# Kernel optimization log

Measured on AMD Instinct MI355X. Metric: run time of the kernel, lower is better.

The kernel has to match this reference:

```python
import jax, jax.numpy as jnp
import numpy as np

N_IN = 512
N_OUT = 256
T = 2048
B = 32


def setup_inputs() -> dict:
    key = jax.random.key(0)
    ks = jax.random.split(key, 9)
    s_in = 1.0 / np.sqrt(N_IN)
    inp = {
        "xt": jax.random.normal(ks[0], (T, B, N_IN), dtype=jnp.float32),
        "ct_forward": jax.random.normal(ks[1], (1, B, N_OUT), dtype=jnp.float32),
        # weights stored torch-style as [out, in]
        "Wx": jax.random.uniform(ks[2], (N_OUT, N_IN), jnp.float32, -s_in, s_in),
        "Wf": jax.random.uniform(ks[3], (N_OUT, N_IN), jnp.float32, -s_in, s_in),
        "bf": jax.random.uniform(ks[4], (N_OUT,), jnp.float32, -s_in, s_in),
        "Wr": jax.random.uniform(ks[5], (N_OUT, N_IN), jnp.float32, -s_in, s_in),
        "br": jax.random.uniform(ks[6], (N_OUT,), jnp.float32, -s_in, s_in),
        "Wc": jax.random.uniform(ks[7], (N_OUT, N_IN), jnp.float32, -s_in, s_in),
        "bc": jax.random.uniform(ks[8], (N_OUT,), jnp.float32, -s_in, s_in),
    }
    return inp


def reference(xt, ct_forward, Wx, Wf, bf, Wr, br, Wc, bc):
    # Batched projections over all timesteps (the GEMM part of SRU).
    x_proj = jnp.einsum("tbi,oi->tbo", xt, Wx)              # [T,B,n_out]
    f = jax.nn.sigmoid(jnp.einsum("tbi,oi->tbo", xt, Wf) + bf)
    r = jax.nn.sigmoid(jnp.einsum("tbi,oi->tbo", xt, Wr) + br)
    cx = jnp.einsum("tbi,oi->tbo", xt, Wc) + bc

    def step(c, inp):
        x_t, ft, rt, cxt = inp
        c = ft * c + (1.0 - ft) * x_t
        h = rt * jnp.tanh(c) + (1.0 - rt) * cxt
        return c, h

    c_final, ht = jax.lax.scan(step, ct_forward[0], (x_proj, f, r, cx))
    # dropout=0.0 -> identity; forward returns (ht, ct)
    return ht, c_final
```

## Files before the change

kernel.cpp:

```cpp
#include <hip/hip_runtime.h>
#include <stdint.h>

#define T_STEPS 2048
#define BATCH   32
#define NIN     512
#define NOUT    256
#define MROWS   (T_STEPS*BATCH)
#define BO      (BATCH*NOUT)
#define NCHUNK  32
#define CHLEN   (T_STEPS/NCHUNK)

typedef _Float16 f16x8 __attribute__((ext_vector_type(8)));
typedef _Float16 f16x4 __attribute__((ext_vector_type(4)));
typedef float    fx4   __attribute__((ext_vector_type(4)));

#define LDSP(p) ((__attribute__((address_space(3))) void*)(p))
#define GLBP(p) ((const __attribute__((address_space(1))) void*)(p))

#define BAR()        asm volatile("s_barrier" ::: "memory")
#define WAITLGKM0()  do { asm volatile("s_waitcnt lgkmcnt(0)" ::: "memory"); __builtin_amdgcn_sched_barrier(0); } while(0)
#define WAITVM(n)    do { asm volatile("s_waitcnt vmcnt(" #n ")" ::: "memory"); __builtin_amdgcn_sched_barrier(0); } while(0)

__global__ __launch_bounds__(256) void convert_w(
    const float* __restrict__ Wx, const float* __restrict__ Wf,
    const float* __restrict__ Wr, const float* __restrict__ Wc,
    _Float16* __restrict__ Wcat)
{
    int idx = blockIdx.x * 256 + threadIdx.x;
    int n  = idx >> 7;
    int k4 = (idx & 127) * 4;
    int g = n >> 8, o = n & 255;
    const float* W = (g == 0) ? Wx : (g == 1) ? Wf : (g == 2) ? Wr : Wc;
    float4 v = *(const float4*)(W + o * NIN + k4);
    f16x4 h;
    h[0] = (_Float16)v.x; h[1] = (_Float16)v.y;
    h[2] = (_Float16)v.z; h[3] = (_Float16)v.w;
    *(f16x4*)(Wcat + n * NIN + k4) = h;
}

#define BM 256
#define BN 256
#define BK 64
#define NGT 32

__global__ __launch_bounds__(512, 1) void gemm_proj(
    const float*    __restrict__ xt,
    const _Float16* __restrict__ Wcat,
    const float* __restrict__ bfv, const float* __restrict__ brv, const float* __restrict__ bcv,
    _Float16* __restrict__ xp_h, _Float16* __restrict__ f_h,
    _Float16* __restrict__ r_h,  _Float16* __restrict__ cx_h)
{
    __shared__ char lds[131072];

    const int tid  = threadIdx.x;
    const int lane = tid & 63;
    const int w    = tid >> 6;
    const int wrq  = w >> 2;
    const int wcq  = w & 3;
    const int lr = lane & 15, lk = lane >> 4;

    int wg = (blockIdx.x & 7) * 32 + (blockIdx.x >> 3);
    const int  cg   = wg & 3;
    const int  mgrp = wg >> 2;
    const long m0 = (long)mgrp * 1024;
    const int  n0 = cg * BN;

    const char* baseAg = (const char*)xt + (m0 + (tid >> 4)) * 2048 + (tid & 15) * 16;
    const int awbase = (tid >> 4) * 128 + (((tid & 15) * 8) ^ (((tid >> 4) & 7) << 4));

    const int rl8  = lane >> 3;
    const int scol = (((lane & 7) ^ rl8) << 4);
    const char* baseB = (const char*)Wcat + ((long)(n0 + w * 8 + rl8)) * 1024 + scol;

    float4 av_h0[4], av_h1[4];
#define ALOAD_H(gi, half, dst) do {                                          \
        const char* _b = baseAg + (long)((gi) >> 3) * 524288                 \
                         + ((gi) & 7) * 256 + (half) * 262144;               \
        _Pragma("unroll")                                                    \
        for (int jj = 0; jj < 4; ++jj)                                       \
            dst[jj] = *(const float4*)(_b + jj * 65536);                     \
    } while (0)
#define AWRITE_H(gi, half, src) do {                                         \
        char* _d = lds + ((gi) & 1) * 32768 + (half) * 16384 + awbase;       \
        _Pragma("unroll")                                                    \
        for (int jj = 0; jj < 4; ++jj) {                                     \
            f16x4 _h;                                                        \
            _h[0] = (_Float16)src[jj].x; _h[1] = (_Float16)src[jj].y;        \
            _h[2] = (_Float16)src[jj].z; _h[3] = (_Float16)src[jj].w;        \
            *(f16x4*)(_d + jj * 4096) = _h;                                  \
        }                                                                    \
    } while (0)
#define STAGE_B(g, h) do {                                                   \
        char* _d = lds + 65536 + ((g) & 1) * 32768 + (h) * 16384 + w * 1024; \
        const char* _s = baseB + ((g) & 7) * 128 + (long)(h) * 131072;       \
        __builtin_amdgcn_global_load_lds(GLBP(_s),         LDSP(_d),        16, 0, 0); \
        __builtin_amdgcn_global_load_lds(GLBP(_s + 65536), LDSP(_d + 8192), 16, 0, 0); \
    } while (0)

    fx4 acc[2][2][4][2];
    #pragma unroll
    for (int a = 0; a < 2; ++a)
        #pragma unroll
        for (int b = 0; b < 2; ++b)
            #pragma unroll
            for (int c = 0; c < 4; ++c)
                #pragma unroll
                for (int d = 0; d < 2; ++d)
                    acc[a][b][c][d] = (fx4){0.f, 0.f, 0.f, 0.f};

    f16x8 Ar[4][2];
    f16x8 B0r[2][2];
    f16x8 B1r[2][2];

#define READ_A(c2, h) do {                                                   \
        _Pragma("unroll")                                                    \
        for (int mf = 0; mf < 4; ++mf) {                                     \
            int rl = wrq * 64 + mf * 16 + lr;                                \
            int rb = (c2) * 32768 + (h) * 16384 + rl * 128;                  \
            _Pragma("unroll")                                                \
            for (int kk = 0; kk < 2; ++kk)                                   \
                Ar[mf][kk] = *(const f16x8*)(lds + rb +                      \
                    ((kk * 64 + lk * 16) ^ ((rl & 7) << 4)));                \
        }                                                                    \
    } while (0)
#define READ_B(c2, h, dst) do {                                              \
        _Pragma("unroll")                                                    \
        for (int nf = 0; nf < 2; ++nf) {                                     \
            int rl = wcq * 32 + nf * 16 + lr;                                \
            int rb = 65536 + (c2) * 32768 + (h) * 16384 + rl * 128;          \
            _Pragma("unroll")                                                \
            for (int kk = 0; kk < 2; ++kk)                                   \
                dst[nf][kk] = *(const f16x8*)(lds + rb +                     \
                    ((kk * 64 + lk * 16) ^ ((rl & 7) << 4)));                \
        }                                                                    \
    } while (0)
#define MMACC(Qr, Qc, Br) do {                                               \
        __builtin_amdgcn_s_setprio(1);                                       \
        _Pragma("unroll")                                                    \
        for (int kk = 0; kk < 2; ++kk)                                       \
            _Pragma("unroll")                                                \
            for (int mf = 0; mf < 4; ++mf)                                   \
                _Pragma("unroll")                                            \
                for (int nf = 0; nf < 2; ++nf)                               \
                    acc[Qr][Qc][mf][nf] = __builtin_amdgcn_mfma_f32_16x16x32_f16( \
                        Br[nf][kk], Ar[mf][kk], acc[Qr][Qc][mf][nf], 0, 0, 0);    \
        __builtin_amdgcn_s_setprio(0);                                       \
    } while (0)

    const int g_out = cg;
    _Float16* outp = (g_out == 0) ? xp_h : (g_out == 1) ? f_h : (g_out == 2) ? r_h : cx_h;
    const float* bias = (g_out == 1) ? bfv : (g_out == 2) ? brv : (g_out == 3) ? bcv : nullptr;

    ALOAD_H(0, 0, av_h0); ALOAD_H(0, 1, av_h1);
    STAGE_B(0, 0); STAGE_B(0, 1);
    WAITVM(4);
    AWRITE_H(0, 0, av_h0); AWRITE_H(0, 1, av_h1);
    ALOAD_H(1, 0, av_h0); ALOAD_H(1, 1, av_h1);
    WAITVM(8);
    WAITLGKM0();
    BAR();

    for (int g = 0; g < NGT; ++g) {
        const int c2 = g & 1;
        READ_A(c2, 0);
        READ_B(c2, 0, B0r);
        if (g + 1 < NGT) STAGE_B(g + 1, 0);
        WAITLGKM0();
        MMACC(0, 0, B0r);
        READ_B(c2, 1, B1r);
        if (g + 1 < NGT) STAGE_B(g + 1, 1);
        WAITLGKM0();
        MMACC(0, 1, B1r);
        READ_A(c2, 1);
        WAITLGKM0();
        MMACC(1, 0, B0r);
        MMACC(1, 1, B1r);
        WAITVM(0);
        if (g + 1 < NGT) {
            AWRITE_H(g + 1, 0, av_h0);
            AWRITE_H(g + 1, 1, av_h1);
            if (g + 2 < NGT) {
                ALOAD_H(g + 2, 0, av_h0);
                ALOAD_H(g + 2, 1, av_h1);
            }
        }
        WAITLGKM0();
        BAR();
        if ((g & 7) == 7) {
            const long mbase = m0 + (long)(g >> 3) * 256;
            #pragma unroll
            for (int Qr = 0; Qr < 2; ++Qr) {
                #pragma unroll
                for (int Qc = 0; Qc < 2; ++Qc) {
                    #pragma unroll
                    for (int nf = 0; nf < 2; ++nf) {
                        const int ob = Qc * 128 + wcq * 32 + nf * 16 + lk * 4;
                        float4 bv4 = (g_out == 0) ? (float4){0.f, 0.f, 0.f, 0.f}
                                                  : *(const float4*)(bias + ob);
                        #pragma unroll
                        for (int mf = 0; mf < 4; ++mf) {
                            long row = mbase + Qr * 128 + wrq * 64 + mf * 16 + lr;
                            fx4 v = acc[Qr][Qc][mf][nf];
                            f16x4 hv;
                            if (g_out == 1 || g_out == 2) {
                                float p0 = v[0] + bv4.x, p1 = v[1] + bv4.y;
                                float p2 = v[2] + bv4.z, p3 = v[3] + bv4.w;
                                hv[0] = (_Float16)(__builtin_amdgcn_rcpf(1.0f + __expf(-p0)));
                                hv[1] = (_Float16)(__builtin_amdgcn_rcpf(1.0f + __expf(-p1)));
                                hv[2] = (_Float16)(__builtin_amdgcn_rcpf(1.0f + __expf(-p2)));
                                hv[3] = (_Float16)(__builtin_amdgcn_rcpf(1.0f + __expf(-p3)));
                            } else {
                                hv[0] = (_Float16)(v[0] + bv4.x);
                                hv[1] = (_Float16)(v[1] + bv4.y);
                                hv[2] = (_Float16)(v[2] + bv4.z);
                                hv[3] = (_Float16)(v[3] + bv4.w);
                            }
                            *(f16x4*)(outp + row * NOUT + ob) = hv;
                            acc[Qr][Qc][mf][nf] = (fx4){0.f, 0.f, 0.f, 0.f};
                        }
                    }
                }
            }
        }
    }
}

__global__ __launch_bounds__(256) void chunk_scan_a(
    const _Float16* __restrict__ f_h, const _Float16* __restrict__ xp_h,
    float* __restrict__ chunkA, float* __restrict__ chunkB)
{
    int tid2 = blockIdx.x * 256 + threadIdx.x;
    int ch = tid2 >> 11;
    int b4 = (tid2 & 2047) << 2;
    long base = (long)ch * CHLEN * BO + b4;
    fx4 a = (fx4){1.f, 1.f, 1.f, 1.f};
    fx4 cc = (fx4){0.f, 0.f, 0.f, 0.f};
    for (int s = 0; s < CHLEN; ++s) {
        long i = base + (long)s * BO;
        f16x4 fv = *(const f16x4*)(f_h + i);
        f16x4 xv = *(const f16x4*)(xp_h + i);
        #pragma unroll
        for (int q = 0; q < 4; ++q) {
            float f = (float)fv[q], x = (float)xv[q];
            cc[q] = f * cc[q] + (1.f - f) * x;
            a[q] *= f;
        }
    }
    *(fx4*)(chunkA + ch * BO + b4) = a;
    *(fx4*)(chunkB + ch * BO + b4) = cc;
}

__global__ __launch_bounds__(256) void chunk_prop(
    const float* __restrict__ ct0,
    const float* __restrict__ chunkA, const float* __restrict__ chunkB,
    float* __restrict__ cin, float* __restrict__ c_final)
{
    int bo = blockIdx.x * 256 + threadIdx.x;
    float c = ct0[bo];
    #pragma unroll
    for (int ch = 0; ch < NCHUNK; ++ch) {
        cin[ch * BO + bo] = c;
        c = chunkA[ch * BO + bo] * c + chunkB[ch * BO + bo];
    }
    c_final[bo] = c;
}

__global__ __launch_bounds__(256) void chunk_scan_h(
    const _Float16* __restrict__ xp_h, const _Float16* __restrict__ f_h,
    const _Float16* __restrict__ r_h,  const _Float16* __restrict__ cx_h,
    const float* __restrict__ cin, float* __restrict__ ht)
{
    int tid2 = blockIdx.x * 256 + threadIdx.x;
    int ch = tid2 >> 11;
    int b4 = (tid2 & 2047) << 2;
    long base = (long)ch * CHLEN * BO + b4;
    fx4 c = *(const fx4*)(cin + ch * BO + b4);
    for (int s = 0; s < CHLEN; ++s) {
        long i = base + (long)s * BO;
        f16x4 fv  = *(const f16x4*)(f_h + i);
        f16x4 xv  = *(const f16x4*)(xp_h + i);
        f16x4 rv  = *(const f16x4*)(r_h + i);
        f16x4 cxv = *(const f16x4*)(cx_h + i);
        fx4 h4;
        #pragma unroll
        for (int q = 0; q < 4; ++q) {
            float f = (float)fv[q], x = (float)xv[q];
            float r = (float)rv[q], cx = (float)cxv[q];
            c[q] = f * c[q] + (1.f - f) * x;
            float e = __expf(2.f * c[q]);
            float th = (e - 1.f) * __builtin_amdgcn_rcpf(e + 1.f);
            h4[q] = r * th + (1.f - r) * cx;
        }
        *(fx4*)(ht + i) = h4;
    }
}

extern "C" void kernel_launch(void* const* d_in, const int* in_sizes, int n_in,
                              void* d_out, int out_size, void* d_ws, size_t ws_size,
                              hipStream_t stream) {
    const float* xt  = (const float*)d_in[0];
    const float* ct0 = (const float*)d_in[1];
    const float* Wx  = (const float*)d_in[2];
    const float* Wf  = (const float*)d_in[3];
    const float* bf_ = (const float*)d_in[4];
    const float* Wr  = (const float*)d_in[5];
    const float* br_ = (const float*)d_in[6];
    const float* Wc  = (const float*)d_in[7];
    const float* bc_ = (const float*)d_in[8];

    float* ht      = (float*)d_out;
    float* c_final = ht + (size_t)MROWS * NOUT;

    char* ws = (char*)d_ws;
    _Float16* Wcat = (_Float16*)ws;
    _Float16* xp_h = (_Float16*)(ws + (1 << 20));
    _Float16* f_h  = xp_h + (size_t)MROWS * NOUT;
    _Float16* r_h  = f_h  + (size_t)MROWS * NOUT;
    _Float16* cx_h = r_h  + (size_t)MROWS * NOUT;
    float* chunkA  = (float*)(cx_h + (size_t)MROWS * NOUT);
    float* chunkB  = chunkA + NCHUNK * BO;
    float* cin     = chunkB + NCHUNK * BO;

    convert_w<<<512, 256, 0, stream>>>(Wx, Wf, Wr, Wc, Wcat);
    gemm_proj<<<256, 512, 0, stream>>>(
        xt, Wcat, bf_, br_, bc_, xp_h, f_h, r_h, cx_h);
    chunk_scan_a<<<256, 256, 0, stream>>>(f_h, xp_h, chunkA, chunkB);
    chunk_prop<<<BO / 256, 256, 0, stream>>>(ct0, chunkA, chunkB, cin, c_final);
    chunk_scan_h<<<256, 256, 0, stream>>>(xp_h, f_h, r_h, cx_h, cin, ht);
}
```

Before: 175.3 us.

## Switch GEMM to 128x128 tiles with 2 blocks per CU and non-persistent grid

Replaces the persistent 256x256-tile GEMM (256 blocks of 512 threads, each walking 4 row tiles) with a conventional grid of 128x128 tiles, 256 threads per block and two blocks per CU. Each block loads its A rows once, computes a single tile and writes the epilogue at the end. The aim is higher occupancy and better latency hiding through concurrent blocks. The cost is less operand reuse per tile: the fp32 A row block is now re-read and re-converted by all eight column-group blocks instead of four, which adds global traffic. The main loop is also simplified into one MFMA phase per k-step.

```diff
diff --git a/kernel.cpp b/kernel.cpp
--- a/kernel.cpp
+++ b/kernel.cpp
@@ -38,31 +38,31 @@
     *(f16x4*)(Wcat + n * NIN + k4) = h;
 }
 
-#define BM 256
-#define BN 256
+#define BM 128
+#define BN 128
 #define BK 64
-#define NGT 32
-
-__global__ __launch_bounds__(512, 1) void gemm_proj(
+#define NGT 8
+
+__global__ __launch_bounds__(256, 2) void gemm_proj(
     const float*    __restrict__ xt,
     const _Float16* __restrict__ Wcat,
     const float* __restrict__ bfv, const float* __restrict__ brv, const float* __restrict__ bcv,
     _Float16* __restrict__ xp_h, _Float16* __restrict__ f_h,
     _Float16* __restrict__ r_h,  _Float16* __restrict__ cx_h)
 {
-    __shared__ char lds[131072];
+    __shared__ char lds[65536];
 
     const int tid  = threadIdx.x;
     const int lane = tid & 63;
     const int w    = tid >> 6;
-    const int wrq  = w >> 2;
-    const int wcq  = w & 3;
+    const int wrq  = w >> 1;
+    const int wcq  = w & 1;
     const int lr = lane & 15, lk = lane >> 4;
 
-    int wg = (blockIdx.x & 7) * 32 + (blockIdx.x >> 3);
-    const int  cg   = wg & 3;
-    const int  mgrp = wg >> 2;
-    const long m0 = (long)mgrp * 1024;
+    int wg = (blockIdx.x & 7) * 512 + (blockIdx.x >> 3);
+    const int  rowblk = wg >> 3;
+    const int  cg     = wg & 7;
+    const long m0 = (long)rowblk * BM;
     const int  n0 = cg * BN;
 
     const char* baseAg = (const char*)xt + (m0 + (tid >> 4)) * 2048 + (tid & 15) * 16;
@@ -72,155 +72,128 @@
     const int scol = (((lane & 7) ^ rl8) << 4);
     const char* baseB = (const char*)Wcat + ((long)(n0 + w * 8 + rl8)) * 1024 + scol;
 
-    float4 av_h0[4], av_h1[4];
-#define ALOAD_H(gi, half, dst) do {                                          \
-        const char* _b = baseAg + (long)((gi) >> 3) * 524288                 \
-                         + ((gi) & 7) * 256 + (half) * 262144;               \
-        _Pragma("unroll")                                                    \
-        for (int jj = 0; jj < 4; ++jj)                                       \
-            dst[jj] = *(const float4*)(_b + jj * 65536);                     \
-    } while (0)
-#define AWRITE_H(gi, half, src) do {                                         \
-        char* _d = lds + ((gi) & 1) * 32768 + (half) * 16384 + awbase;       \
-        _Pragma("unroll")                                                    \
-        for (int jj = 0; jj < 4; ++jj) {                                     \
+    float4 av[8];
+#define ALOAD(gi) do {                                                       \
+        const char* _b = baseAg + ((gi) & 7) * 256;                          \
+        _Pragma("unroll")                                                    \
+        for (int jj = 0; jj < 8; ++jj)                                       \
+            av[jj] = *(const float4*)(_b + jj * 32768);                      \
+    } while (0)
+#define AWRITE(gi) do {                                                      \
+        char* _d = lds + ((gi) & 1) * 16384 + awbase;                        \
+        _Pragma("unroll")                                                    \
+        for (int jj = 0; jj < 8; ++jj) {                                     \
             f16x4 _h;                                                        \
-            _h[0] = (_Float16)src[jj].x; _h[1] = (_Float16)src[jj].y;        \
-            _h[2] = (_Float16)src[jj].z; _h[3] = (_Float16)src[jj].w;        \
-            *(f16x4*)(_d + jj * 4096) = _h;                                  \
+            _h[0] = (_Float16)av[jj].x; _h[1] = (_Float16)av[jj].y;          \
+            _h[2] = (_Float16)av[jj].z; _h[3] = (_Float16)av[jj].w;          \
+            *(f16x4*)(_d + jj * 2048) = _h;                                  \
         }                                                                    \
     } while (0)
 #define STAGE_B(g, h) do {                                                   \
-        char* _d = lds + 65536 + ((g) & 1) * 32768 + (h) * 16384 + w * 1024; \
-        const char* _s = baseB + ((g) & 7) * 128 + (long)(h) * 131072;       \
+        char* _d = lds + 32768 + ((g) & 1) * 16384 + (h) * 8192 + w * 1024;  \
+        const char* _s = baseB + ((g) & 7) * 128 + (long)(h) * 65536;        \
         __builtin_amdgcn_global_load_lds(GLBP(_s),         LDSP(_d),        16, 0, 0); \
-        __builtin_amdgcn_global_load_lds(GLBP(_s + 65536), LDSP(_d + 8192), 16, 0, 0); \
-    } while (0)
-
-    fx4 acc[2][2][4][2];
+        __builtin_amdgcn_global_load_lds(GLBP(_s + 32768), LDSP(_d + 4096), 16, 0, 0); \
+    } while (0)
+
+    fx4 acc[4][4];
     #pragma unroll
-    for (int a = 0; a < 2; ++a)
+    for (int i = 0; i < 4; ++i)
         #pragma unroll
-        for (int b = 0; b < 2; ++b)
-            #pragma unroll
-            for (int c = 0; c < 4; ++c)
-                #pragma unroll
-                for (int d = 0; d < 2; ++d)
-                    acc[a][b][c][d] = (fx4){0.f, 0.f, 0.f, 0.f};
+        for (int j = 0; j < 4; ++j) acc[i][j] = (fx4){0.f, 0.f, 0.f, 0.f};
 
     f16x8 Ar[4][2];
-    f16x8 B0r[2][2];
-    f16x8 B1r[2][2];
-
-#define READ_A(c2, h) do {                                                   \
+    f16x8 Br[4][2];
+
+#define READ_A(c2) do {                                                      \
         _Pragma("unroll")                                                    \
         for (int mf = 0; mf < 4; ++mf) {                                     \
             int rl = wrq * 64 + mf * 16 + lr;                                \
-            int rb = (c2) * 32768 + (h) * 16384 + rl * 128;                  \
+            int rb = (c2) * 16384 + rl * 128;                                \
             _Pragma("unroll")                                                \
             for (int kk = 0; kk < 2; ++kk)                                   \
                 Ar[mf][kk] = *(const f16x8*)(lds + rb +                      \
                     ((kk * 64 + lk * 16) ^ ((rl & 7) << 4)));                \
         }                                                                    \
     } while (0)
-#define READ_B(c2, h, dst) do {                                              \
-        _Pragma("unroll")                                                    \
-        for (int nf = 0; nf < 2; ++nf) {                                     \
-            int rl = wcq * 32 + nf * 16 + lr;                                \
-            int rb = 65536 + (c2) * 32768 + (h) * 16384 + rl * 128;          \
+#define READ_B(c2) do {                                                      \
+        _Pragma("unroll")                                                    \
+        for (int nf = 0; nf < 4; ++nf) {                                     \
+            int rl = wcq * 64 + nf * 16 + lr;                                \
+            int rb = 32768 + (c2) * 16384 + rl * 128;                        \
             _Pragma("unroll")                                                \
             for (int kk = 0; kk < 2; ++kk)                                   \
-                dst[nf][kk] = *(const f16x8*)(lds + rb +                     \
+                Br[nf][kk] = *(const f16x8*)(lds + rb +                      \
                     ((kk * 64 + lk * 16) ^ ((rl & 7) << 4)));                \
         }                                                                    \
     } while (0)
-#define MMACC(Qr, Qc, Br) do {                                               \
+#define MMACC_ALL() do {                                                     \
         __builtin_amdgcn_s_setprio(1);                                       \
         _Pragma("unroll")                                                    \
         for (int kk = 0; kk < 2; ++kk)                                       \
             _Pragma("unroll")                                                \
             for (int mf = 0; mf < 4; ++mf)                                   \
                 _Pragma("unroll")                                            \
-                for (int nf = 0; nf < 2; ++nf)                               \
-                    acc[Qr][Qc][mf][nf] = __builtin_amdgcn_mfma_f32_16x16x32_f16( \
-                        Br[nf][kk], Ar[mf][kk], acc[Qr][Qc][mf][nf], 0, 0, 0);    \
+                for (int nf = 0; nf < 4; ++nf)                               \
+                    acc[mf][nf] = __builtin_amdgcn_mfma_f32_16x16x32_f16(    \
+                        Br[nf][kk], Ar[mf][kk], acc[mf][nf], 0, 0, 0);       \
         __builtin_amdgcn_s_setprio(0);                                       \
     } while (0)
 
-    const int g_out = cg;
+    const int g_out = cg >> 1;
+    const int obase = (cg & 1) * 128;
     _Float16* outp = (g_out == 0) ? xp_h : (g_out == 1) ? f_h : (g_out == 2) ? r_h : cx_h;
     const float* bias = (g_out == 1) ? bfv : (g_out == 2) ? brv : (g_out == 3) ? bcv : nullptr;
 
-    ALOAD_H(0, 0, av_h0); ALOAD_H(0, 1, av_h1);
+    ALOAD(0);
     STAGE_B(0, 0); STAGE_B(0, 1);
     WAITVM(4);
-    AWRITE_H(0, 0, av_h0); AWRITE_H(0, 1, av_h1);
-    ALOAD_H(1, 0, av_h0); ALOAD_H(1, 1, av_h1);
+    AWRITE(0);
+    ALOAD(1);
     WAITVM(8);
     WAITLGKM0();
     BAR();
 
     for (int g = 0; g < NGT; ++g) {
         const int c2 = g & 1;
-        READ_A(c2, 0);
-        READ_B(c2, 0, B0r);
-        if (g + 1 < NGT) STAGE_B(g + 1, 0);
+        if (g + 1 < NGT) { STAGE_B(g + 1, 0); STAGE_B(g + 1, 1); }
+        READ_A(c2);
+        READ_B(c2);
         WAITLGKM0();
-        MMACC(0, 0, B0r);
-        READ_B(c2, 1, B1r);
-        if (g + 1 < NGT) STAGE_B(g + 1, 1);
-        WAITLGKM0();
-        MMACC(0, 1, B1r);
-        READ_A(c2, 1);
-        WAITLGKM0();
-        MMACC(1, 0, B0r);
-        MMACC(1, 1, B1r);
+        MMACC_ALL();
         WAITVM(0);
         if (g + 1 < NGT) {
-            AWRITE_H(g + 1, 0, av_h0);
-            AWRITE_H(g + 1, 1, av_h1);
-            if (g + 2 < NGT) {
-                ALOAD_H(g + 2, 0, av_h0);
-                ALOAD_H(g + 2, 1, av_h1);
-            }
+            AWRITE(g + 1);
+            if (g + 2 < NGT) ALOAD(g + 2);
         }
         WAITLGKM0();
         BAR();
-        if ((g & 7) == 7) {
-            const long mbase = m0 + (long)(g >> 3) * 256;
-            #pragma unroll
-            for (int Qr = 0; Qr < 2; ++Qr) {
-                #pragma unroll
-                for (int Qc = 0; Qc < 2; ++Qc) {
-                    #pragma unroll
-                    for (int nf = 0; nf < 2; ++nf) {
-                        const int ob = Qc * 128 + wcq * 32 + nf * 16 + lk * 4;
-                        float4 bv4 = (g_out == 0) ? (float4){0.f, 0.f, 0.f, 0.f}
-                                                  : *(const float4*)(bias + ob);
-                        #pragma unroll
-                        for (int mf = 0; mf < 4; ++mf) {
-                            long row = mbase + Qr * 128 + wrq * 64 + mf * 16 + lr;
-                            fx4 v = acc[Qr][Qc][mf][nf];
-                            f16x4 hv;
-                            if (g_out == 1 || g_out == 2) {
-                                float p0 = v[0] + bv4.x, p1 = v[1] + bv4.y;
-                                float p2 = v[2] + bv4.z, p3 = v[3] + bv4.w;
-                                hv[0] = (_Float16)(__builtin_amdgcn_rcpf(1.0f + __expf(-p0)));
-                                hv[1] = (_Float16)(__builtin_amdgcn_rcpf(1.0f + __expf(-p1)));
-                                hv[2] = (_Float16)(__builtin_amdgcn_rcpf(1.0f + __expf(-p2)));
-                                hv[3] = (_Float16)(__builtin_amdgcn_rcpf(1.0f + __expf(-p3)));
-                            } else {
-                                hv[0] = (_Float16)(v[0] + bv4.x);
-                                hv[1] = (_Float16)(v[1] + bv4.y);
-                                hv[2] = (_Float16)(v[2] + bv4.z);
-                                hv[3] = (_Float16)(v[3] + bv4.w);
-                            }
-                            *(f16x4*)(outp + row * NOUT + ob) = hv;
-                            acc[Qr][Qc][mf][nf] = (fx4){0.f, 0.f, 0.f, 0.f};
-                        }
-                    }
-                }
+    }
+
+    #pragma unroll
+    for (int nf = 0; nf < 4; ++nf) {
+        const int ob = obase + wcq * 64 + nf * 16 + lk * 4;
+        float4 bv4 = (g_out == 0) ? (float4){0.f, 0.f, 0.f, 0.f}
+                                  : *(const float4*)(bias + ob);
+        #pragma unroll
+        for (int mf = 0; mf < 4; ++mf) {
+            long row = m0 + wrq * 64 + mf * 16 + lr;
+            fx4 v = acc[mf][nf];
+            f16x4 hv;
+            if (g_out == 1 || g_out == 2) {
+                float p0 = v[0] + bv4.x, p1 = v[1] + bv4.y;
+                float p2 = v[2] + bv4.z, p3 = v[3] + bv4.w;
+                hv[0] = (_Float16)(__builtin_amdgcn_rcpf(1.0f + __expf(-p0)));
+                hv[1] = (_Float16)(__builtin_amdgcn_rcpf(1.0f + __expf(-p1)));
+                hv[2] = (_Float16)(__builtin_amdgcn_rcpf(1.0f + __expf(-p2)));
+                hv[3] = (_Float16)(__builtin_amdgcn_rcpf(1.0f + __expf(-p3)));
+            } else {
+                hv[0] = (_Float16)(v[0] + bv4.x);
+                hv[1] = (_Float16)(v[1] + bv4.y);
+                hv[2] = (_Float16)(v[2] + bv4.z);
+                hv[3] = (_Float16)(v[3] + bv4.w);
             }
+            *(f16x4*)(outp + row * NOUT + ob) = hv;
         }
     }
 }
@@ -322,7 +295,7 @@
     float* cin     = chunkB + NCHUNK * BO;
 
     convert_w<<<512, 256, 0, stream>>>(Wx, Wf, Wr, Wc, Wcat);
-    gemm_proj<<<256, 512, 0, stream>>>(
+    gemm_proj<<<(MROWS / BM) * 8, 256, 0, stream>>>(
         xt, Wcat, bf_, br_, bc_, xp_h, f_h, r_h, cx_h);
     chunk_scan_a<<<256, 256, 0, stream>>>(f_h, xp_h, chunkA, chunkB);
     chunk_prop<<<BO / 256, 256, 0, stream>>>(ct0, chunkA, chunkB, cin, c_final);
```

New measurement: 204.5 us. 16.6% more time.
